# Kernel tuning notes

Measured on AMD Instinct MI355X. Metric: run time of the kernel, lower is better.

The kernel has to match this reference:

```python
import jax, jax.numpy as jnp
import numpy as np

N = 50000      # nodes
E = 800000     # edges (avg degree 16)
D = 128        # input_nf = output_nf
H = 128        # hidden_nf


def _lin_init(key, fan_in, fan_out, gain=1.0):
    return gain * jax.random.normal(key, (fan_in, fan_out), jnp.float32) / np.sqrt(fan_in)


def setup_inputs() -> dict:
    key = jax.random.key(0)
    ks = jax.random.split(key, 20)
    h = jax.random.normal(ks[0], (N, D), jnp.float32)
    coord_diff = 0.5 * jax.random.normal(ks[1], (E, 3), jnp.float32)
    row = jax.random.randint(ks[2], (E,), 0, N, jnp.int32)
    col = jax.random.randint(ks[3], (E,), 0, N, jnp.int32)
    return {
        "h": h, "coord_diff": coord_diff, "row": row, "col": col,
        # edge_nn: Linear(2D+1 -> H), SiLU, Linear(H -> H), SiLU
        "We1": _lin_init(ks[4], 2 * D + 1, H), "be1": jnp.zeros((H,), jnp.float32),
        "We2": _lin_init(ks[5], H, H),          "be2": jnp.zeros((H,), jnp.float32),
        # node_nn: Linear(H+D -> H), SiLU, Linear(H -> D)
        "Wn1": _lin_init(ks[6], H + D, H), "bn1": jnp.zeros((H,), jnp.float32),
        "Wn2": _lin_init(ks[7], H, D),     "bn2": jnp.zeros((D,), jnp.float32),
        # coord_nn: Linear(H -> H), SiLU, Linear(H -> 1, no bias, gain 0.001)
        "Wc1": _lin_init(ks[8], H, H), "bc1": jnp.zeros((H,), jnp.float32),
        "Wc2": _lin_init(ks[9], H, 1, gain=0.001),
        # vel_scaling_nn: Linear(D -> H), SiLU, Linear(H -> 1)
        "Wv1": _lin_init(ks[10], D, H), "bv1": jnp.zeros((H,), jnp.float32),
        "Wv2": _lin_init(ks[11], H, 1), "bv2": jnp.zeros((1,), jnp.float32),
    }


def reference(h, coord_diff, row, col,
              We1, be1, We2, be2,
              Wn1, bn1, Wn2, bn2,
              Wc1, bc1, Wc2,
              Wv1, bv1, Wv2, bv2):
    n = h.shape[0]
    silu = jax.nn.silu
    # radial: squared edge length, [E,1]
    radial = jnp.sum(coord_diff * coord_diff, axis=1, keepdims=True)
    # edge model: gather endpoint features + radial, 2-layer SiLU MLP
    e_in = jnp.concatenate([h[row], h[col], radial], axis=1)        # [E, 2D+1]
    m = silu(silu(e_in @ We1 + be1) @ We2 + be2)                    # [E, H]
    # force model: per-edge scalar coefficient, clamped scatter-mean (coords_weight=1.0)
    coef = silu(m @ Wc1 + bc1) @ Wc2                                # [E, 1]
    trans = jnp.clip(coord_diff * coef, -100.0, 100.0)              # [E, 3]
    f_sum = jax.ops.segment_sum(trans, row, num_segments=n)         # [N, 3]
    cnt = jax.ops.segment_sum(jnp.ones((trans.shape[0], 1), trans.dtype), row, num_segments=n)
    force = f_sum / jnp.clip(cnt, 1.0)                              # segment mean, count clamped >=1
    # node model: scatter-sum of edge messages, then 2-layer MLP
    agg = jax.ops.segment_sum(m, row, num_segments=n)               # [N, H]
    h_cat = jnp.concatenate([h, agg], axis=1)                       # [N, D+H]
    h_out = silu(h_cat @ Wn1 + bn1) @ Wn2 + bn2                     # [N, D]
    # velocity scaling head
    vel = silu(h @ Wv1 + bv1) @ Wv2 + bv2                           # [N, 1]
    return (vel, force, h_out)
```

## Files before the change

### kernel.cpp

```cpp
#include <hip/hip_runtime.h>

#define NN 50000
#define EE 800000

typedef unsigned short u16;
typedef unsigned int u32;
typedef __attribute__((ext_vector_type(8))) short short8;
typedef __attribute__((ext_vector_type(4))) float f32x4;
typedef __attribute__((ext_vector_type(2))) float f32x2;

__device__ __forceinline__ u16 f2bf(float f) {
    union { float f; u32 i; } v; v.f = f;
    u32 x = v.i;
    return (u16)((x + 0x7fffu + ((x >> 16) & 1u)) >> 16);
}
__device__ __forceinline__ u32 pkr(float lo, float hi) {
    union { float f; u32 i; } a, b; a.f = lo; b.f = hi;
    return __builtin_amdgcn_perm(b.i + 0x8000u, a.i + 0x8000u, 0x07060302u);
}
__device__ __forceinline__ float bf2f(short x) {
    union { u32 i; float f; } v; v.i = ((u32)(u16)x) << 16; return v.f;
}
__device__ __forceinline__ float siluf(float x) {
    return x * __builtin_amdgcn_rcpf(1.0f + __expf(-x));
}
__device__ __forceinline__ void atomic_pk_add_bf16(u16* addr, u32 data) {
    asm volatile("global_atomic_pk_add_bf16 %0, %1, off" :: "v"(addr), "v"(data) : "memory");
}

__device__ __forceinline__ int b_idx2(int k, int n) {
    int chunk = ((k >> 5) << 3) + ((n >> 5) << 1) + (n & 1);
    return chunk * 512 + (((k >> 3) & 3) << 7) + (((n >> 1) & 15) << 3) + (k & 7);
}

__global__ __launch_bounds__(256) void prep_kernel(
    const float* __restrict__ We1, const float* __restrict__ We2,
    const float* __restrict__ Wc1, const float* __restrict__ Wn1,
    const float* __restrict__ Wn2, const float* __restrict__ Wv1,
    u16* __restrict__ We1bf, u16* __restrict__ We2bf, u16* __restrict__ Wc1bf,
    u16* __restrict__ Wn1bf, u16* __restrict__ Wn2bf, u16* __restrict__ Wv1bf)
{
    int i = blockIdx.x * 256 + threadIdx.x;
    if (i < 32768) {
        int k = i >> 7, n = i & 127;
        We1bf[b_idx2(k, n)] = f2bf(We1[k * 128 + n]);
    } else if (i < 49152) {
        int t = i - 32768; int k = t >> 7, n = t & 127;
        We2bf[b_idx2(k, n)] = f2bf(We2[k * 128 + n]);
    } else if (i < 65536) {
        int t = i - 49152; int k = t >> 7, n = t & 127;
        Wc1bf[b_idx2(k, n)] = f2bf(Wc1[k * 128 + n]);
    } else if (i < 98304) {
        int t = i - 65536; int k = t >> 7, n = t & 127;
        Wn1bf[b_idx2(k, n)] = f2bf(Wn1[k * 128 + n]);
    } else if (i < 114688) {
        int t = i - 98304; int k = t >> 7, n = t & 127;
        Wn2bf[b_idx2(k, n)] = f2bf(Wn2[k * 128 + n]);
    } else {
        int t = i - 114688; int k = t >> 7, n = t & 127;
        Wv1bf[b_idx2(k, n)] = f2bf(Wv1[k * 128 + n]);
    }
}

__global__ __launch_bounds__(256) void hist_kernel(const int* __restrict__ row,
                                                   u32* __restrict__ bins)
{
    int e = blockIdx.x * 256 + threadIdx.x;
    if (e < EE) atomicAdd(&bins[row[e]], 1u);
}

__global__ __launch_bounds__(256) void scan1_kernel(const u32* __restrict__ bins,
                                                    u32* __restrict__ part)
{
    __shared__ u32 wsum[4];
    int i = blockIdx.x * 256 + threadIdx.x;
    u32 v = (i < NN) ? bins[i] : 0u;
    #pragma unroll
    for (int o = 1; o < 64; o <<= 1) v += __shfl_xor(v, o);
    if ((threadIdx.x & 63) == 0) wsum[threadIdx.x >> 6] = v;
    __syncthreads();
    if (threadIdx.x == 0) part[blockIdx.x] = wsum[0] + wsum[1] + wsum[2] + wsum[3];
}

__global__ __launch_bounds__(256) void scan2_kernel(u32* __restrict__ part, int np)
{
    __shared__ u32 s[256];
    int t = threadIdx.x;
    s[t] = (t < np) ? part[t] : 0u;
    __syncthreads();
    if (t == 0) {
        u32 run = 0;
        for (int i = 0; i < 256; ++i) { u32 x = s[i]; s[i] = run; run += x; }
    }
    __syncthreads();
    if (t < np) part[t] = s[t];
}

__global__ __launch_bounds__(256) void scan3_kernel(const u32* __restrict__ bins,
                                                    const u32* __restrict__ part,
                                                    u32* __restrict__ cursor)
{
    __shared__ u32 wsum[4];
    int t = threadIdx.x;
    int i = blockIdx.x * 256 + t;
    u32 v = (i < NN) ? bins[i] : 0u;
    u32 x = v;
    #pragma unroll
    for (int o = 1; o < 64; o <<= 1) {
        u32 y = __shfl_up(x, o);
        if ((t & 63) >= o) x += y;
    }
    if ((t & 63) == 63) wsum[t >> 6] = x;
    __syncthreads();
    u32 base = part[blockIdx.x];
    for (int wv = 0; wv < (t >> 6); ++wv) base += wsum[wv];
    if (i < NN) cursor[i] = base + x - v;
}

__global__ __launch_bounds__(256) void scatter_kernel(
    const int* __restrict__ row, const int* __restrict__ col,
    const float* __restrict__ cdiff, u32* __restrict__ cursor,
    u32* __restrict__ edata)
{
    int e = blockIdx.x * 256 + threadIdx.x;
    if (e < EE) {
        int r = row[e];
        u32 p = atomicAdd(&cursor[r], 1u);
        float cx = cdiff[(size_t)e * 3 + 0];
        float cy = cdiff[(size_t)e * 3 + 1];
        float cz = cdiff[(size_t)e * 3 + 2];
        float rad = cx * cx + cy * cy + cz * cz;
        uint4 ed;
        ed.x = (u32)r;
        ed.y = (u32)col[e];
        ed.z = __float_as_uint(rad);
        ed.w = (u32)e;
        *(uint4*)(edata + (size_t)p * 4) = ed;
    }
}

__global__ __launch_bounds__(256, 4) void pgemm_kernel(
    const float* __restrict__ h, const float* __restrict__ be1,
    const u16* __restrict__ We1bf,
    u16* __restrict__ P1bf, u16* __restrict__ P2bf,
    u16* __restrict__ hbf, u32 use_hbf)
{
    __shared__ u16 sX[8192];

    const int tid = threadIdx.x;
    const int nblk = blockIdx.x * 64;
    const int w = tid >> 6;
    const int lane = tid & 63;
    const int m15 = lane & 15, q = lane >> 4;
    const int n0 = w * 32 + 2 * m15, n1 = n0 + 1;
    const int ard = (m15 + 64 * q) * 8;
    const float b0 = be1[n0], b1 = be1[n1];

    {
        int r = tid & 63, j = tid >> 6;
        int n = nblk + r; if (n > NN - 1) n = NN - 1;
        const float* src = h + (size_t)n * 128 + j * 32;
        #pragma unroll
        for (int i = 0; i < 4; ++i) {
            float4 a = *(const float4*)(src + i * 8);
            float4 b = *(const float4*)(src + i * 8 + 4);
            int slot = r + ((j * 4 + i) << 6);
            uint4 v = make_uint4(pkr(a.x, a.y), pkr(a.z, a.w),
                                 pkr(b.x, b.y), pkr(b.z, b.w));
            *(uint4*)&sX[slot * 8] = v;
            if (use_hbf)
                *(uint4*)(hbf + (size_t)n * 128 + j * 32 + i * 8) = v;
        }
    }
    __syncthreads();

    f32x4 acc[4][2];

    #pragma unroll
    for (int mt = 0; mt < 4; ++mt)
        #pragma unroll
        for (int r = 0; r < 4; ++r) { acc[mt][0][r] = b0; acc[mt][1][r] = b1; }
    #pragma unroll
    for (int c = 0; c < 4; ++c) {
        short8 bf0 = *(const short8*)(We1bf + (c * 8 + w * 2 + 0) * 512 + lane * 8);
        short8 bf1 = *(const short8*)(We1bf + (c * 8 + w * 2 + 1) * 512 + lane * 8);
        #pragma unroll
        for (int mt = 0; mt < 4; ++mt) {
            short8 af = *(const short8*)(sX + ard + c * 2048 + mt * 128);
            acc[mt][0] = __builtin_amdgcn_mfma_f32_16x16x32_bf16(af, bf0, acc[mt][0], 0, 0, 0);
            acc[mt][1] = __builtin_amdgcn_mfma_f32_16x16x32_bf16(af, bf1, acc[mt][1], 0, 0, 0);
        }
    }
    #pragma unroll
    for (int mt = 0; mt < 4; ++mt)
        #pragma unroll
        for (int r = 0; r < 4; ++r) {
            int n = nblk + mt * 16 + q * 4 + r;
            if (n < NN)
                *(u32*)(P1bf + (size_t)n * 128 + n0) = pkr(acc[mt][0][r], acc[mt][1][r]);
        }

    #pragma unroll
    for (int mt = 0; mt < 4; ++mt)
        #pragma unroll
        for (int r = 0; r < 4; ++r) { acc[mt][0][r] = 0.0f; acc[mt][1][r] = 0.0f; }
    #pragma unroll
    for (int c = 4; c < 8; ++c) {
        short8 bf0 = *(const short8*)(We1bf + (c * 8 + w * 2 + 0) * 512 + lane * 8);
        short8 bf1 = *(const short8*)(We1bf + (c * 8 + w * 2 + 1) * 512 + lane * 8);
        #pragma unroll
        for (int mt = 0; mt < 4; ++mt) {
            short8 af = *(const short8*)(sX + ard + (c - 4) * 2048 + mt * 128);
            acc[mt][0] = __builtin_amdgcn_mfma_f32_16x16x32_bf16(af, bf0, acc[mt][0], 0, 0, 0);
            acc[mt][1] = __builtin_amdgcn_mfma_f32_16x16x32_bf16(af, bf1, acc[mt][1], 0, 0, 0);
        }
    }
    #pragma unroll
    for (int mt = 0; mt < 4; ++mt)
        #pragma unroll
        for (int r = 0; r < 4; ++r) {
            int n = nblk + mt * 16 + q * 4 + r;
            if (n < NN)
                *(u32*)(P2bf + (size_t)n * 128 + n0) = pkr(acc[mt][0][r], acc[mt][1][r]);
        }
}

__global__ __launch_bounds__(256, 8) void edge_kernel(
    const u16* __restrict__ P1bf, const u16* __restrict__ P2bf,
    const float* __restrict__ cdiff,
    const u32* __restrict__ edata,
    const float* __restrict__ We1,
    const float* __restrict__ be2, const float* __restrict__ bc1,
    const float* __restrict__ Wc2,
    const u16* __restrict__ We2bf, const u16* __restrict__ Wc1bf,
    u16* __restrict__ aggbf, float* __restrict__ fsum)
{
    __shared__ u16 sT[8192];
    __shared__ int sRow[64];
    __shared__ int sEg[64];
    __shared__ int sRid[64];
    __shared__ float sCoefP[4][64];
    __shared__ float sF[192];

    const int tid = threadIdx.x;
    const int e0 = blockIdx.x * 64;
    const int w = tid >> 6;
    const int lane = tid & 63;
    const int m15 = lane & 15, q = lane >> 4;
    const int n0 = w * 32 + 2 * m15, n1 = n0 + 1;
    const int lsw = (lane ^ q) * 8;
    const int a_ = m15 >> 2;
    const int sbase = (a_ << 7) + (q << 5) + ((m15 & 3) << 1);
    const int o0 = (0 ^ a_) << 3, o1 = (1 ^ a_) << 3, o2 = (2 ^ a_) << 3, o3 = (3 ^ a_) << 3;

    const float b2a = be2[n0], b2b = be2[n1];
    const float b3a = bc1[n0], b3b = bc1[n1];
    const float wc2a = Wc2[n0], wc2b = Wc2[n1];

    {
        int e = tid & 63, seg = tid >> 6;
        uint4 ed = *(const uint4*)(edata + (size_t)(e0 + e) * 4);
        int nr = (int)ed.x, nc = (int)ed.y;
        float rad = __uint_as_float(ed.z);
        if (seg == 0) { sRow[e] = nr; sEg[e] = (int)ed.w; }
        const u16* p1 = P1bf + (size_t)nr * 128 + seg * 32;
        const u16* p2 = P2bf + (size_t)nc * 128 + seg * 32;
        const float* wr = We1 + 256 * 128 + seg * 32;
        u16* tb = sT + (((seg * 4 + (e >> 4)) << 9) + (((e >> 2) & 3) << 5));
        const int rl = e & 3;
        #pragma unroll 2
        for (int g = 0; g < 4; ++g) {
            short8 x1 = *(const short8*)(p1 + g * 8);
            short8 x2 = *(const short8*)(p2 + g * 8);
            float4 wa = *(const float4*)(wr + g * 8);
            float4 wb = *(const float4*)(wr + g * 8 + 4);
            float v[8];
            #pragma unroll
            for (int t = 0; t < 4; ++t) {
                v[t]     = siluf(bf2f(x1[t])     + bf2f(x2[t])     + rad * ((const float*)&wa)[t]);
                v[t + 4] = siluf(bf2f(x1[t + 4]) + bf2f(x2[t + 4]) + rad * ((const float*)&wb)[t]);
            }
            uint4 dd = make_uint4(pkr(v[0], v[1]), pkr(v[2], v[3]),
                                  pkr(v[4], v[5]), pkr(v[6], v[7]));
            *(uint4*)(tb + ((g << 7) + ((rl ^ g) << 3))) = dd;
        }
    }
    __syncthreads();

    if (tid < 64) {
        int e = tid;
        int head = (e == 0) || (sRow[e] != sRow[e - 1]);
        int v = head ? e : 0;
        #pragma unroll
        for (int o = 1; o < 64; o <<= 1) {
            int y = __shfl_up(v, o);
            if (e >= o && y > v) v = y;
        }
        sRid[e] = v;
        sF[e * 3 + 0] = 0.f; sF[e * 3 + 1] = 0.f; sF[e * 3 + 2] = 0.f;
    }

    f32x4 acc[4][2];
    u32 d[4][4];

    #pragma unroll
    for (int mt = 0; mt < 4; ++mt)
        #pragma unroll
        for (int r = 0; r < 4; ++r) { acc[mt][0][r] = b2a; acc[mt][1][r] = b2b; }
    #pragma unroll
    for (int c = 0; c < 4; ++c) {
        short8 bf0 = *(const short8*)(We2bf + (c * 8 + w * 2 + 0) * 512 + lane * 8);
        short8 bf1 = *(const short8*)(We2bf + (c * 8 + w * 2 + 1) * 512 + lane * 8);
        #pragma unroll
        for (int mt = 0; mt < 4; ++mt) {
            short8 af = *(const short8*)(sT + (c * 4 + mt) * 512 + lsw);
            acc[mt][0] = __builtin_amdgcn_mfma_f32_16x16x32_bf16(af, bf0, acc[mt][0], 0, 0, 0);
            acc[mt][1] = __builtin_amdgcn_mfma_f32_16x16x32_bf16(af, bf1, acc[mt][1], 0, 0, 0);
        }
    }
    #pragma unroll
    for (int mt = 0; mt < 4; ++mt)
        #pragma unroll
        for (int r = 0; r < 4; ++r)
            d[mt][r] = pkr(siluf(acc[mt][0][r]), siluf(acc[mt][1][r]));
    __syncthreads();
    #pragma unroll
    for (int mt = 0; mt < 4; ++mt) {
        u16* bp = sT + (w * 4 + mt) * 512 + sbase;
        *(u32*)(bp + o0) = d[mt][0];
        *(u32*)(bp + o1) = d[mt][1];
        *(u32*)(bp + o2) = d[mt][2];
        *(u32*)(bp + o3) = d[mt][3];
    }
    __syncthreads();

    #pragma unroll
    for (int mt = 0; mt < 4; ++mt)
        #pragma unroll
        for (int r = 0; r < 4; ++r) { acc[mt][0][r] = b3a; acc[mt][1][r] = b3b; }
    #pragma unroll
    for (int c = 0; c < 4; ++c) {
        short8 bf0 = *(const short8*)(Wc1bf + (c * 8 + w * 2 + 0) * 512 + lane * 8);
        short8 bf1 = *(const short8*)(Wc1bf + (c * 8 + w * 2 + 1) * 512 + lane * 8);
        #pragma unroll
        for (int mt = 0; mt < 4; ++mt) {
            short8 af = *(const short8*)(sT + (c * 4 + mt) * 512 + lsw);
            acc[mt][0] = __builtin_amdgcn_mfma_f32_16x16x32_bf16(af, bf0, acc[mt][0], 0, 0, 0);
            acc[mt][1] = __builtin_amdgcn_mfma_f32_16x16x32_bf16(af, bf1, acc[mt][1], 0, 0, 0);
        }
    }
    #pragma unroll
    for (int mt = 0; mt < 4; ++mt)
        #pragma unroll
        for (int r = 0; r < 4; ++r) {
            float pv = fmaf(siluf(acc[mt][0][r]), wc2a, siluf(acc[mt][1][r]) * wc2b);
            pv += __shfl_xor(pv, 1);
            pv += __shfl_xor(pv, 2);
            pv += __shfl_xor(pv, 4);
            pv += __shfl_xor(pv, 8);
            if (m15 == 0) sCoefP[w][mt * 16 + q * 4 + r] = pv;
        }

    {
        const int P = tid & 63, C = 2 * P, g = tid >> 6;
        const int xorb = (C >> 3) & 3;
        const int base = ((((C >> 5) * 4 + g) << 9)) + (((C >> 3) & 3) << 7) + (C & 7);
        float s0 = 0.f, s1 = 0.f;
        int prow = sRow[g * 16];
        #pragma unroll
        for (int i = 0; i < 16; ++i) {
            u32 v = *(const u32*)(sT + base + (((i >> 2) & 3) << 5) + (((i & 3) ^ xorb) << 3));
            int r = sRow[g * 16 + i];
            if (r != prow) {
                atomic_pk_add_bf16(aggbf + (size_t)prow * 128 + C, pkr(s0, s1));
                s0 = 0.f; s1 = 0.f; prow = r;
            }
            s0 += bf2f((short)(v & 0xffffu));
            s1 += bf2f((short)(v >> 16));
        }
        atomic_pk_add_bf16(aggbf + (size_t)prow * 128 + C, pkr(s0, s1));
    }
    __syncthreads();

    if (tid < 192) {
        int e = tid / 3, ax = tid - e * 3;
        float coef = sCoefP[0][e] + sCoefP[1][e] + sCoefP[2][e] + sCoefP[3][e];
        float tr = cdiff[(size_t)sEg[e] * 3 + ax] * coef;
        tr = fminf(fmaxf(tr, -100.f), 100.f);
        atomicAdd(&sF[sRid[e] * 3 + ax], tr);
    }
    __syncthreads();
    if (tid < 192) {
        int e = tid / 3, ax = tid - e * 3;
        if (e == 0 || sRow[e] != sRow[e - 1])
            atomicAdd(&fsum[(size_t)sRow[e] * 3 + ax], sF[e * 3 + ax]);
    }
}

__global__ __launch_bounds__(256, 4) void node_kernel(
    const float* __restrict__ h, const u16* __restrict__ hbf, u32 use_hbf,
    const float* __restrict__ bn1, const float* __restrict__ bn2,
    const float* __restrict__ bv1, const float* __restrict__ Wv2,
    const float* __restrict__ bv2,
    const u16* __restrict__ Wn1bf, const u16* __restrict__ Wn2bf,
    const u16* __restrict__ Wv1bf,
    const u16* __restrict__ aggbf, const float* __restrict__ fsum,
    const u32* __restrict__ bins, float* __restrict__ out)
{
    __shared__ u16 sX[16384];
    __shared__ float sBn1[128], sBn2[128], sBv1[128];
    __shared__ float sVelP[4][64];
    u16* sT = sX + 8192;

    const int tid = threadIdx.x;
    const int nblk = blockIdx.x * 64;
    const int w = tid >> 6;
    const int lane = tid & 63;
    const int m15 = lane & 15, q = lane >> 4;
    const int n0 = w * 32 + 2 * m15, n1 = n0 + 1;
    const int lsw = (lane ^ q) * 8;
    const int a_ = m15 >> 2;
    const int sbase = (a_ << 7) + (q << 5) + ((m15 & 3) << 1);
    const int o0 = (0 ^ a_) << 3, o1 = (1 ^ a_) << 3, o2 = (2 ^ a_) << 3, o3 = (3 ^ a_) << 3;
    const int ard = (m15 + 64 * q) * 8;

    if (tid < 192) {
        int r = tid / 3, ax = tid - r * 3;
        int n = nblk + r;
        if (n < NN)
            out[NN + (size_t)n * 3 + ax] = fsum[(size_t)n * 3 + ax] * __builtin_amdgcn_rcpf(fmaxf((float)bins[n], 1.0f));
    }
    if (tid < 128) { sBn1[tid] = bn1[tid]; sBn2[tid] = bn2[tid]; sBv1[tid] = bv1[tid]; }
    const float wv2a = Wv2[n0], wv2b = Wv2[n1];

    {
        int r = tid & 63, j = tid >> 6;
        int n = nblk + r; if (n > NN - 1) n = NN - 1;
        if (j < 2) {
            if (use_hbf) {
                const u16* src = hbf + (size_t)n * 128 + j * 64;
                #pragma unroll
                for (int i = 0; i < 8; ++i) {
                    int slot = r + ((j * 8 + i) << 6);
                    *(uint4*)&sX[slot * 8] = *(const uint4*)(src + i * 8);
                }
            } else {
                const float* src = h + (size_t)n * 128 + j * 64;
                #pragma unroll
                for (int i = 0; i < 8; ++i) {
                    float4 a = *(const float4*)(src + i * 8);
                    float4 b = *(const float4*)(src + i * 8 + 4);
                    int slot = r + ((j * 8 + i) << 6);
                    *(uint4*)&sX[slot * 8] = make_uint4(pkr(a.x, a.y), pkr(a.z, a.w),
                                                        pkr(b.x, b.y), pkr(b.z, b.w));
                }
            }
        } else {
            const u16* src = aggbf + (size_t)n * 128 + (j & 1) * 64;
            #pragma unroll
            for (int i = 0; i < 8; ++i) {
                int slot = r + ((j * 8 + i) << 6);
                *(uint4*)&sX[slot * 8] = *(const uint4*)(src + i * 8);
            }
        }
    }
    __syncthreads();

    f32x4 acc[4][2];

    {
        float b0 = sBn1[n0], b1 = sBn1[n1];
        #pragma unroll
        for (int mt = 0; mt < 4; ++mt)
            #pragma unroll
            for (int r = 0; r < 4; ++r) { acc[mt][0][r] = b0; acc[mt][1][r] = b1; }
    }
    #pragma unroll
    for (int c = 0; c < 8; ++c) {
        short8 bf0 = *(const short8*)(Wn1bf + (c * 8 + w * 2 + 0) * 512 + lane * 8);
        short8 bf1 = *(const short8*)(Wn1bf + (c * 8 + w * 2 + 1) * 512 + lane * 8);
        #pragma unroll
        for (int mt = 0; mt < 4; ++mt) {
            short8 af = *(const short8*)(sX + ard + c * 2048 + mt * 128);
            acc[mt][0] = __builtin_amdgcn_mfma_f32_16x16x32_bf16(af, bf0, acc[mt][0], 0, 0, 0);
            acc[mt][1] = __builtin_amdgcn_mfma_f32_16x16x32_bf16(af, bf1, acc[mt][1], 0, 0, 0);
        }
    }
    u32 dn[4][4];
    #pragma unroll
    for (int mt = 0; mt < 4; ++mt)
        #pragma unroll
        for (int r = 0; r < 4; ++r)
            dn[mt][r] = pkr(siluf(acc[mt][0][r]), siluf(acc[mt][1][r]));
    __syncthreads();
    #pragma unroll
    for (int mt = 0; mt < 4; ++mt) {
        u16* bp = sT + (w * 4 + mt) * 512 + sbase;
        *(u32*)(bp + o0) = dn[mt][0];
        *(u32*)(bp + o1) = dn[mt][1];
        *(u32*)(bp + o2) = dn[mt][2];
        *(u32*)(bp + o3) = dn[mt][3];
    }
    __syncthreads();

    {
        float b0 = sBn2[n0], b1 = sBn2[n1];
        #pragma unroll
        for (int mt = 0; mt < 4; ++mt)
            #pragma unroll
            for (int r = 0; r < 4; ++r) { acc[mt][0][r] = b0; acc[mt][1][r] = b1; }
    }
    #pragma unroll
    for (int c = 0; c < 4; ++c) {
        short8 bf0 = *(const short8*)(Wn2bf + (c * 8 + w * 2 + 0) * 512 + lane * 8);
        short8 bf1 = *(const short8*)(Wn2bf + (c * 8 + w * 2 + 1) * 512 + lane * 8);
        #pragma unroll
        for (int mt = 0; mt < 4; ++mt) {
            short8 af = *(const short8*)(sT + (c * 4 + mt) * 512 + lsw);
            acc[mt][0] = __builtin_amdgcn_mfma_f32_16x16x32_bf16(af, bf0, acc[mt][0], 0, 0, 0);
            acc[mt][1] = __builtin_amdgcn_mfma_f32_16x16x32_bf16(af, bf1, acc[mt][1], 0, 0, 0);
        }
    }
    #pragma unroll
    for (int mt = 0; mt < 4; ++mt)
        #pragma unroll
        for (int r = 0; r < 4; ++r) {
            int n = nblk + mt * 16 + q * 4 + r;
            if (n < NN) {
                f32x2 v; v.x = acc[mt][0][r]; v.y = acc[mt][1][r];
                *(f32x2*)(out + (size_t)4 * NN + (size_t)n * 128 + n0) = v;
            }
        }

    {
        float b0 = sBv1[n0], b1 = sBv1[n1];
        #pragma unroll
        for (int mt = 0; mt < 4; ++mt)
            #pragma unroll
            for (int r = 0; r < 4; ++r) { acc[mt][0][r] = b0; acc[mt][1][r] = b1; }
    }
    #pragma unroll
    for (int c = 0; c < 4; ++c) {
        short8 bf0 = *(const short8*)(Wv1bf + (c * 8 + w * 2 + 0) * 512 + lane * 8);
        short8 bf1 = *(const short8*)(Wv1bf + (c * 8 + w * 2 + 1) * 512 + lane * 8);
        #pragma unroll
        for (int mt = 0; mt < 4; ++mt) {
            short8 af = *(const short8*)(sX + ard + c * 2048 + mt * 128);
            acc[mt][0] = __builtin_amdgcn_mfma_f32_16x16x32_bf16(af, bf0, acc[mt][0], 0, 0, 0);
            acc[mt][1] = __builtin_amdgcn_mfma_f32_16x16x32_bf16(af, bf1, acc[mt][1], 0, 0, 0);
        }
    }
    #pragma unroll
    for (int mt = 0; mt < 4; ++mt)
        #pragma unroll
        for (int r = 0; r < 4; ++r) {
            float pv = fmaf(siluf(acc[mt][0][r]), wv2a, siluf(acc[mt][1][r]) * wv2b);
            pv += __shfl_xor(pv, 1);
            pv += __shfl_xor(pv, 2);
            pv += __shfl_xor(pv, 4);
            pv += __shfl_xor(pv, 8);
            if (m15 == 0) sVelP[w][mt * 16 + q * 4 + r] = pv;
        }
    __syncthreads();

    if (tid < 64) {
        int n = nblk + tid;
        if (n < NN)
            out[n] = bv2[0] + sVelP[0][tid] + sVelP[1][tid] + sVelP[2][tid] + sVelP[3][tid];
    }
}

extern "C" void kernel_launch(void* const* d_in, const int* in_sizes, int n_in,
                              void* d_out, int out_size, void* d_ws, size_t ws_size,
                              hipStream_t stream) {
    const float* h     = (const float*)d_in[0];
    const float* cdiff = (const float*)d_in[1];
    const int* row     = (const int*)d_in[2];
    const int* col     = (const int*)d_in[3];
    const float* We1 = (const float*)d_in[4];
    const float* be1 = (const float*)d_in[5];
    const float* We2 = (const float*)d_in[6];
    const float* be2 = (const float*)d_in[7];
    const float* Wn1 = (const float*)d_in[8];
    const float* bn1 = (const float*)d_in[9];
    const float* Wn2 = (const float*)d_in[10];
    const float* bn2 = (const float*)d_in[11];
    const float* Wc1 = (const float*)d_in[12];
    const float* bc1 = (const float*)d_in[13];
    const float* Wc2 = (const float*)d_in[14];
    const float* Wv1 = (const float*)d_in[15];
    const float* bv1 = (const float*)d_in[16];
    const float* Wv2 = (const float*)d_in[17];
    const float* bv2 = (const float*)d_in[18];

    u16* aggbf  = (u16*)d_ws;
    float* fsum = (float*)(aggbf + (size_t)NN * 128);
    u32* bins   = (u32*)(fsum + (size_t)NN * 3);
    u16* We1bf = (u16*)(bins + NN);
    u16* We2bf = We1bf + 32768;
    u16* Wc1bf = We2bf + 16384;
    u16* Wn1bf = Wc1bf + 16384;
    u16* Wn2bf = Wn1bf + 32768;
    u16* Wv1bf = Wn2bf + 16384;
    u16* P1bf  = Wv1bf + 16384;
    float* out = (float*)d_out;

    const size_t base_bytes = (size_t)26662144;
    u16* hbf = (u16*)((char*)d_ws + base_bytes);
    u32 use_hbf = (ws_size >= base_bytes + (size_t)NN * 256) ? 1u : 0u;

    u32* cursor = (u32*)out;
    u32* part   = cursor + NN;
    u16* P2bf   = (u16*)(out + (size_t)4 * NN);
    u32* edata  = (u32*)(P2bf + (size_t)NN * 128);

    size_t zero_bytes = (size_t)NN * 128 * 2 + (size_t)NN * 3 * 4 + (size_t)NN * 4;
    hipMemsetAsync(d_ws, 0, zero_bytes, stream);

    const int NSC = (NN + 255) / 256;

    prep_kernel<<<512, 256, 0, stream>>>(We1, We2, Wc1, Wn1, Wn2, Wv1,
                                         We1bf, We2bf, Wc1bf, Wn1bf, Wn2bf, Wv1bf);
    pgemm_kernel<<<(NN + 63) / 64, 256, 0, stream>>>(h, be1, We1bf, P1bf, P2bf,
                                                     hbf, use_hbf);
    hist_kernel<<<(EE + 255) / 256, 256, 0, stream>>>(row, bins);
    scan1_kernel<<<NSC, 256, 0, stream>>>(bins, part);
    scan2_kernel<<<1, 256, 0, stream>>>(part, NSC);
    scan3_kernel<<<NSC, 256, 0, stream>>>(bins, part, cursor);
    scatter_kernel<<<(EE + 255) / 256, 256, 0, stream>>>(row, col, cdiff, cursor, edata);
    edge_kernel<<<EE / 64, 256, 0, stream>>>(P1bf, P2bf, cdiff, edata,
                                             We1, be2, bc1, Wc2,
                                             We2bf, Wc1bf,
                                             aggbf, fsum);
    node_kernel<<<(NN + 63) / 64, 256, 0, stream>>>(h, hbf, use_hbf,
                                                    bn1, bn2, bv1, Wv2, bv2,
                                                    Wn1bf, Wn2bf, Wv1bf,
                                                    aggbf, fsum, bins, out);
}
```

Before: 392.3 us.

## Move velocity head into pgemm and halve node tiles to 32 rows

The velocity MLP (h@Wv1, SiLU, dot Wv2) moves from node_kernel into pgemm_kernel, reusing the bf16 h tile already staged in shared memory there. The cursor scratch buffer is shifted past the vel slot in the output so the early vel write is not overwritten. Both pgemm and node kernels now process 32 nodes per block instead of 64, doubling grid size and halving shared memory per block. This trims node_kernel's tail work and raises occupancy, at the cost of less weight reuse per block.

Result: faster. 377.1 us (-3.9%).

```diff
diff --git a/kernel.cpp b/kernel.cpp
--- a/kernel.cpp
+++ b/kernel.cpp
@@ -141,43 +141,46 @@
 
 __global__ __launch_bounds__(256, 4) void pgemm_kernel(
     const float* __restrict__ h, const float* __restrict__ be1,
-    const u16* __restrict__ We1bf,
+    const float* __restrict__ bv1, const float* __restrict__ Wv2,
+    const float* __restrict__ bv2,
+    const u16* __restrict__ We1bf, const u16* __restrict__ Wv1bf,
     u16* __restrict__ P1bf, u16* __restrict__ P2bf,
-    u16* __restrict__ hbf, u32 use_hbf)
-{
-    __shared__ u16 sX[8192];
+    u16* __restrict__ hbf, u32 use_hbf, float* __restrict__ vel)
+{
+    __shared__ u16 sX[4096];
+    __shared__ float sVelP[4][32];
 
     const int tid = threadIdx.x;
-    const int nblk = blockIdx.x * 64;
+    const int nblk = blockIdx.x * 32;
     const int w = tid >> 6;
     const int lane = tid & 63;
     const int m15 = lane & 15, q = lane >> 4;
     const int n0 = w * 32 + 2 * m15, n1 = n0 + 1;
-    const int ard = (m15 + 64 * q) * 8;
+    const int ard = (m15 + 32 * q) * 8;
     const float b0 = be1[n0], b1 = be1[n1];
 
     {
-        int r = tid & 63, j = tid >> 6;
+        int r = tid & 31, j = tid >> 5;
         int n = nblk + r; if (n > NN - 1) n = NN - 1;
-        const float* src = h + (size_t)n * 128 + j * 32;
-        #pragma unroll
-        for (int i = 0; i < 4; ++i) {
-            float4 a = *(const float4*)(src + i * 8);
-            float4 b = *(const float4*)(src + i * 8 + 4);
-            int slot = r + ((j * 4 + i) << 6);
+        #pragma unroll
+        for (int i = 0; i < 2; ++i) {
+            int kg = j * 2 + i;
+            const float* src = h + (size_t)n * 128 + kg * 8;
+            float4 a = *(const float4*)(src);
+            float4 b = *(const float4*)(src + 4);
             uint4 v = make_uint4(pkr(a.x, a.y), pkr(a.z, a.w),
                                  pkr(b.x, b.y), pkr(b.z, b.w));
-            *(uint4*)&sX[slot * 8] = v;
+            *(uint4*)&sX[(r + 32 * kg) * 8] = v;
             if (use_hbf)
-                *(uint4*)(hbf + (size_t)n * 128 + j * 32 + i * 8) = v;
-        }
-    }
-    __syncthreads();
-
-    f32x4 acc[4][2];
-
-    #pragma unroll
-    for (int mt = 0; mt < 4; ++mt)
+                *(uint4*)(hbf + (size_t)n * 128 + kg * 8) = v;
+        }
+    }
+    __syncthreads();
+
+    f32x4 acc[2][2];
+
+    #pragma unroll
+    for (int mt = 0; mt < 2; ++mt)
         #pragma unroll
         for (int r = 0; r < 4; ++r) { acc[mt][0][r] = b0; acc[mt][1][r] = b1; }
     #pragma unroll
@@ -185,14 +188,14 @@
         short8 bf0 = *(const short8*)(We1bf + (c * 8 + w * 2 + 0) * 512 + lane * 8);
         short8 bf1 = *(const short8*)(We1bf + (c * 8 + w * 2 + 1) * 512 + lane * 8);
         #pragma unroll
-        for (int mt = 0; mt < 4; ++mt) {
-            short8 af = *(const short8*)(sX + ard + c * 2048 + mt * 128);
+        for (int mt = 0; mt < 2; ++mt) {
+            short8 af = *(const short8*)(sX + ard + c * 1024 + mt * 128);
             acc[mt][0] = __builtin_amdgcn_mfma_f32_16x16x32_bf16(af, bf0, acc[mt][0], 0, 0, 0);
             acc[mt][1] = __builtin_amdgcn_mfma_f32_16x16x32_bf16(af, bf1, acc[mt][1], 0, 0, 0);
         }
     }
     #pragma unroll
-    for (int mt = 0; mt < 4; ++mt)
+    for (int mt = 0; mt < 2; ++mt)
         #pragma unroll
         for (int r = 0; r < 4; ++r) {
             int n = nblk + mt * 16 + q * 4 + r;
@@ -201,7 +204,7 @@
         }
 
     #pragma unroll
-    for (int mt = 0; mt < 4; ++mt)
+    for (int mt = 0; mt < 2; ++mt)
         #pragma unroll
         for (int r = 0; r < 4; ++r) { acc[mt][0][r] = 0.0f; acc[mt][1][r] = 0.0f; }
     #pragma unroll
@@ -209,20 +212,57 @@
         short8 bf0 = *(const short8*)(We1bf + (c * 8 + w * 2 + 0) * 512 + lane * 8);
         short8 bf1 = *(const short8*)(We1bf + (c * 8 + w * 2 + 1) * 512 + lane * 8);
         #pragma unroll
-        for (int mt = 0; mt < 4; ++mt) {
-            short8 af = *(const short8*)(sX + ard + (c - 4) * 2048 + mt * 128);
+        for (int mt = 0; mt < 2; ++mt) {
+            short8 af = *(const short8*)(sX + ard + (c - 4) * 1024 + mt * 128);
             acc[mt][0] = __builtin_amdgcn_mfma_f32_16x16x32_bf16(af, bf0, acc[mt][0], 0, 0, 0);
             acc[mt][1] = __builtin_amdgcn_mfma_f32_16x16x32_bf16(af, bf1, acc[mt][1], 0, 0, 0);
         }
     }
     #pragma unroll
-    for (int mt = 0; mt < 4; ++mt)
+    for (int mt = 0; mt < 2; ++mt)
         #pragma unroll
         for (int r = 0; r < 4; ++r) {
             int n = nblk + mt * 16 + q * 4 + r;
             if (n < NN)
                 *(u32*)(P2bf + (size_t)n * 128 + n0) = pkr(acc[mt][0][r], acc[mt][1][r]);
         }
+
+    {
+        const float bva = bv1[n0], bvb = bv1[n1];
+        const float wv2a = Wv2[n0], wv2b = Wv2[n1];
+        #pragma unroll
+        for (int mt = 0; mt < 2; ++mt)
+            #pragma unroll
+            for (int r = 0; r < 4; ++r) { acc[mt][0][r] = bva; acc[mt][1][r] = bvb; }
+        #pragma unroll
+        for (int c = 0; c < 4; ++c) {
+            short8 bf0 = *(const short8*)(Wv1bf + (c * 8 + w * 2 + 0) * 512 + lane * 8);
+            short8 bf1 = *(const short8*)(Wv1bf + (c * 8 + w * 2 + 1) * 512 + lane * 8);
+            #pragma unroll
+            for (int mt = 0; mt < 2; ++mt) {
+                short8 af = *(const short8*)(sX + ard + c * 1024 + mt * 128);
+                acc[mt][0] = __builtin_amdgcn_mfma_f32_16x16x32_bf16(af, bf0, acc[mt][0], 0, 0, 0);
+                acc[mt][1] = __builtin_amdgcn_mfma_f32_16x16x32_bf16(af, bf1, acc[mt][1], 0, 0, 0);
+            }
+        }
+        #pragma unroll
+        for (int mt = 0; mt < 2; ++mt)
+            #pragma unroll
+            for (int r = 0; r < 4; ++r) {
+                float pv = fmaf(siluf(acc[mt][0][r]), wv2a, siluf(acc[mt][1][r]) * wv2b);
+                pv += __shfl_xor(pv, 1);
+                pv += __shfl_xor(pv, 2);
+                pv += __shfl_xor(pv, 4);
+                pv += __shfl_xor(pv, 8);
+                if (m15 == 0) sVelP[w][mt * 16 + q * 4 + r] = pv;
+            }
+        __syncthreads();
+        if (tid < 32) {
+            int n = nblk + tid;
+            if (n < NN)
+                vel[n] = bv2[0] + sVelP[0][tid] + sVelP[1][tid] + sVelP[2][tid] + sVelP[3][tid];
+        }
+    }
 }
 
 __global__ __launch_bounds__(256, 8) void edge_kernel(
@@ -400,20 +440,16 @@
 __global__ __launch_bounds__(256, 4) void node_kernel(
     const float* __restrict__ h, const u16* __restrict__ hbf, u32 use_hbf,
     const float* __restrict__ bn1, const float* __restrict__ bn2,
-    const float* __restrict__ bv1, const float* __restrict__ Wv2,
-    const float* __restrict__ bv2,
     const u16* __restrict__ Wn1bf, const u16* __restrict__ Wn2bf,
-    const u16* __restrict__ Wv1bf,
     const u16* __restrict__ aggbf, const float* __restrict__ fsum,
     const u32* __restrict__ bins, float* __restrict__ out)
 {
-    __shared__ u16 sX[16384];
-    __shared__ float sBn1[128], sBn2[128], sBv1[128];
-    __shared__ float sVelP[4][64];
-    u16* sT = sX + 8192;
+    __shared__ u16 sX[8192];
+    __shared__ float sBn1[128], sBn2[128];
+    u16* sT = sX + 4096;
 
     const int tid = threadIdx.x;
-    const int nblk = blockIdx.x * 64;
+    const int nblk = blockIdx.x * 32;
     const int w = tid >> 6;
     const int lane = tid & 63;
     const int m15 = lane & 15, q = lane >> 4;
@@ -422,56 +458,55 @@
     const int a_ = m15 >> 2;
     const int sbase = (a_ << 7) + (q << 5) + ((m15 & 3) << 1);
     const int o0 = (0 ^ a_) << 3, o1 = (1 ^ a_) << 3, o2 = (2 ^ a_) << 3, o3 = (3 ^ a_) << 3;
-    const int ard = (m15 + 64 * q) * 8;
-
-    if (tid < 192) {
+    const int ard = (m15 + 32 * q) * 8;
+
+    if (tid < 96) {
         int r = tid / 3, ax = tid - r * 3;
         int n = nblk + r;
         if (n < NN)
             out[NN + (size_t)n * 3 + ax] = fsum[(size_t)n * 3 + ax] * __builtin_amdgcn_rcpf(fmaxf((float)bins[n], 1.0f));
     }
-    if (tid < 128) { sBn1[tid] = bn1[tid]; sBn2[tid] = bn2[tid]; sBv1[tid] = bv1[tid]; }
-    const float wv2a = Wv2[n0], wv2b = Wv2[n1];
+    if (tid < 128) { sBn1[tid] = bn1[tid]; sBn2[tid] = bn2[tid]; }
 
     {
-        int r = tid & 63, j = tid >> 6;
+        int r = tid & 31, j = tid >> 5;
         int n = nblk + r; if (n > NN - 1) n = NN - 1;
-        if (j < 2) {
+        if (j < 4) {
             if (use_hbf) {
-                const u16* src = hbf + (size_t)n * 128 + j * 64;
                 #pragma unroll
-                for (int i = 0; i < 8; ++i) {
-                    int slot = r + ((j * 8 + i) << 6);
-                    *(uint4*)&sX[slot * 8] = *(const uint4*)(src + i * 8);
+                for (int i = 0; i < 4; ++i) {
+                    int kg = j * 4 + i;
+                    *(uint4*)&sX[(r + 32 * kg) * 8] =
+                        *(const uint4*)(hbf + (size_t)n * 128 + kg * 8);
                 }
             } else {
-                const float* src = h + (size_t)n * 128 + j * 64;
                 #pragma unroll
-                for (int i = 0; i < 8; ++i) {
-                    float4 a = *(const float4*)(src + i * 8);
-                    float4 b = *(const float4*)(src + i * 8 + 4);
-                    int slot = r + ((j * 8 + i) << 6);
-                    *(uint4*)&sX[slot * 8] = make_uint4(pkr(a.x, a.y), pkr(a.z, a.w),
-                                                        pkr(b.x, b.y), pkr(b.z, b.w));
+                for (int i = 0; i < 4; ++i) {
+                    int kg = j * 4 + i;
+                    const float* src = h + (size_t)n * 128 + kg * 8;
+                    float4 a = *(const float4*)(src);
+                    float4 b = *(const float4*)(src + 4);
+                    *(uint4*)&sX[(r + 32 * kg) * 8] = make_uint4(pkr(a.x, a.y), pkr(a.z, a.w),
+                                                                 pkr(b.x, b.y), pkr(b.z, b.w));
                 }
             }
         } else {
-            const u16* src = aggbf + (size_t)n * 128 + (j & 1) * 64;
             #pragma unroll
-            for (int i = 0; i < 8; ++i) {
-                int slot = r + ((j * 8 + i) << 6);
-                *(uint4*)&sX[slot * 8] = *(const uint4*)(src + i * 8);
+            for (int i = 0; i < 4; ++i) {
+                int kg = j * 4 + i;
+                *(uint4*)&sX[(r + 32 * kg) * 8] =
+                    *(const uint4*)(aggbf + (size_t)n * 128 + (kg - 16) * 8);
             }
         }
     }
     __syncthreads();
 
-    f32x4 acc[4][2];
+    f32x4 acc[2][2];
 
     {
         float b0 = sBn1[n0], b1 = sBn1[n1];
         #pragma unroll
-        for (int mt = 0; mt < 4; ++mt)
+        for (int mt = 0; mt < 2; ++mt)
             #pragma unroll
             for (int r = 0; r < 4; ++r) { acc[mt][0][r] = b0; acc[mt][1][r] = b1; }
     }
@@ -480,22 +515,22 @@
         short8 bf0 = *(const short8*)(Wn1bf + (c * 8 + w * 2 + 0) * 512 + lane * 8);
         short8 bf1 = *(const short8*)(Wn1bf + (c * 8 + w * 2 + 1) * 512 + lane * 8);
         #pragma unroll
-        for (int mt = 0; mt < 4; ++mt) {
-            short8 af = *(const short8*)(sX + ard + c * 2048 + mt * 128);
+        for (int mt = 0; mt < 2; ++mt) {
+            short8 af = *(const short8*)(sX + ard + c * 1024 + mt * 128);
             acc[mt][0] = __builtin_amdgcn_mfma_f32_16x16x32_bf16(af, bf0, acc[mt][0], 0, 0, 0);
             acc[mt][1] = __builtin_amdgcn_mfma_f32_16x16x32_bf16(af, bf1, acc[mt][1], 0, 0, 0);
         }
     }
-    u32 dn[4][4];
-    #pragma unroll
-    for (int mt = 0; mt < 4; ++mt)
+    u32 dn[2][4];
+    #pragma unroll
+    for (int mt = 0; mt < 2; ++mt)
         #pragma unroll
         for (int r = 0; r < 4; ++r)
             dn[mt][r] = pkr(siluf(acc[mt][0][r]), siluf(acc[mt][1][r]));
     __syncthreads();
     #pragma unroll
-    for (int mt = 0; mt < 4; ++mt) {
-        u16* bp = sT + (w * 4 + mt) * 512 + sbase;
+    for (int mt = 0; mt < 2; ++mt) {
+        u16* bp = sT + (w * 2 + mt) * 512 + sbase;
         *(u32*)(bp + o0) = dn[mt][0];
         *(u32*)(bp + o1) = dn[mt][1];
         *(u32*)(bp + o2) = dn[mt][2];
@@ -506,7 +541,7 @@
     {
         float b0 = sBn2[n0], b1 = sBn2[n1];
         #pragma unroll
-        for (int mt = 0; mt < 4; ++mt)
+        for (int mt = 0; mt < 2; ++mt)
             #pragma unroll
             for (int r = 0; r < 4; ++r) { acc[mt][0][r] = b0; acc[mt][1][r] = b1; }
     }
@@ -515,14 +550,14 @@
         short8 bf0 = *(const short8*)(Wn2bf + (c * 8 + w * 2 + 0) * 512 + lane * 8);
         short8 bf1 = *(const short8*)(Wn2bf + (c * 8 + w * 2 + 1) * 512 + lane * 8);
         #pragma unroll
-        for (int mt = 0; mt < 4; ++mt) {
-            short8 af = *(const short8*)(sT + (c * 4 + mt) * 512 + lsw);
+        for (int mt = 0; mt < 2; ++mt) {
+            short8 af = *(const short8*)(sT + (c * 2 + mt) * 512 + lsw);
             acc[mt][0] = __builtin_amdgcn_mfma_f32_16x16x32_bf16(af, bf0, acc[mt][0], 0, 0, 0);
             acc[mt][1] = __builtin_amdgcn_mfma_f32_16x16x32_bf16(af, bf1, acc[mt][1], 0, 0, 0);
         }
     }
     #pragma unroll
-    for (int mt = 0; mt < 4; ++mt)
+    for (int mt = 0; mt < 2; ++mt)
         #pragma unroll
         for (int r = 0; r < 4; ++r) {
             int n = nblk + mt * 16 + q * 4 + r;
@@ -531,43 +566,6 @@
                 *(f32x2*)(out + (size_t)4 * NN + (size_t)n * 128 + n0) = v;
             }
         }
-
-    {
-        float b0 = sBv1[n0], b1 = sBv1[n1];
-        #pragma unroll
-        for (int mt = 0; mt < 4; ++mt)
-            #pragma unroll
-            for (int r = 0; r < 4; ++r) { acc[mt][0][r] = b0; acc[mt][1][r] = b1; }
-    }
-    #pragma unroll
-    for (int c = 0; c < 4; ++c) {
-        short8 bf0 = *(const short8*)(Wv1bf + (c * 8 + w * 2 + 0) * 512 + lane * 8);
-        short8 bf1 = *(const short8*)(Wv1bf + (c * 8 + w * 2 + 1) * 512 + lane * 8);
-        #pragma unroll
-        for (int mt = 0; mt < 4; ++mt) {
-            short8 af = *(const short8*)(sX + ard + c * 2048 + mt * 128);
-            acc[mt][0] = __builtin_amdgcn_mfma_f32_16x16x32_bf16(af, bf0, acc[mt][0], 0, 0, 0);
-            acc[mt][1] = __builtin_amdgcn_mfma_f32_16x16x32_bf16(af, bf1, acc[mt][1], 0, 0, 0);
-        }
-    }
-    #pragma unroll
-    for (int mt = 0; mt < 4; ++mt)
-        #pragma unroll
-        for (int r = 0; r < 4; ++r) {
-            float pv = fmaf(siluf(acc[mt][0][r]), wv2a, siluf(acc[mt][1][r]) * wv2b);
-            pv += __shfl_xor(pv, 1);
-            pv += __shfl_xor(pv, 2);
-            pv += __shfl_xor(pv, 4);
-            pv += __shfl_xor(pv, 8);
-            if (m15 == 0) sVelP[w][mt * 16 + q * 4 + r] = pv;
-        }
-    __syncthreads();
-
-    if (tid < 64) {
-        int n = nblk + tid;
-        if (n < NN)
-            out[n] = bv2[0] + sVelP[0][tid] + sVelP[1][tid] + sVelP[2][tid] + sVelP[3][tid];
-    }
 }
 
 extern "C" void kernel_launch(void* const* d_in, const int* in_sizes, int n_in,
@@ -609,7 +607,7 @@
     u16* hbf = (u16*)((char*)d_ws + base_bytes);
     u32 use_hbf = (ws_size >= base_bytes + (size_t)NN * 256) ? 1u : 0u;
 
-    u32* cursor = (u32*)out;
+    u32* cursor = (u32*)(out + NN);
     u32* part   = cursor + NN;
     u16* P2bf   = (u16*)(out + (size_t)4 * NN);
     u32* edata  = (u32*)(P2bf + (size_t)NN * 128);
@@ -621,8 +619,9 @@
 
     prep_kernel<<<512, 256, 0, stream>>>(We1, We2, Wc1, Wn1, Wn2, Wv1,
                                          We1bf, We2bf, Wc1bf, Wn1bf, Wn2bf, Wv1bf);
-    pgemm_kernel<<<(NN + 63) / 64, 256, 0, stream>>>(h, be1, We1bf, P1bf, P2bf,
-                                                     hbf, use_hbf);
+    pgemm_kernel<<<(NN + 31) / 32, 256, 0, stream>>>(h, be1, bv1, Wv2, bv2,
+                                                     We1bf, Wv1bf, P1bf, P2bf,
+                                                     hbf, use_hbf, out);
     hist_kernel<<<(EE + 255) / 256, 256, 0, stream>>>(row, bins);
     scan1_kernel<<<NSC, 256, 0, stream>>>(bins, part);
     scan2_kernel<<<1, 256, 0, stream>>>(part, NSC);
@@ -632,8 +631,8 @@
                                              We1, be2, bc1, Wc2,
                                              We2bf, Wc1bf,
                                              aggbf, fsum);
-    node_kernel<<<(NN + 63) / 64, 256, 0, stream>>>(h, hbf, use_hbf,
-                                                    bn1, bn2, bv1, Wv2, bv2,
-                                                    Wn1bf, Wn2bf, Wv1bf,
+    node_kernel<<<(NN + 31) / 32, 256, 0, stream>>>(h, hbf, use_hbf,
+                                                    bn1, bn2,
+                                                    Wn1bf, Wn2bf,
                                                     aggbf, fsum, bins, out);
 }
```
